# Kernel optimization log

Measured on AMD Instinct MI355X. Metric: run time of the kernel, lower is better.

The kernel has to match this reference:

```python
import jax, jax.numpy as jnp
import numpy as np

B, T = 4, 15
NY = NX = 256
RES = 0.05
LAT0 = 32.0
G = 9.81
F0 = 1e-4
C0 = 2.7
DT = 21600.0
TINT = 86400.0
NSTEP = int(TINT // DT)  # 4 Euler sub-steps

# --- grid spacing: mean of dx, dy as in lonlat2dxdy (uniform lon/lat grid) ---
_lat = LAT0 + RES * np.arange(NX, dtype=np.float64)  # lat varies along axis 1
_dx_mean = RES * 111000.0
_dy_mean = RES * 111000.0 * np.mean(np.cos(np.deg2rad(_lat)))
DX = np.float32(0.5 * (_dx_mean + _dy_mean))

# --- Helmholtz operator in DST-I space, shape (NY-2, NX-2) (square grid) ---
_i = np.arange(1, NX - 1, dtype=np.float64)
_j = np.arange(1, NY - 1, dtype=np.float64)
_X, _Y = np.meshgrid(_i, _j, indexing='ij')
_lap = (2 * (np.cos(np.pi / (NX - 1) * _X) - 1) / DX**2
        + 2 * (np.cos(np.pi / (NY - 1) * _Y) - 1) / DX**2)
HELM = jnp.asarray((G / F0) * _lap - G * F0 / C0**2, dtype=jnp.float32)

# --- boundary masks (SSH=None -> no NaN land mask; ind0 is empty) ---
_m = np.full((NY, NX), 3, dtype=np.int32)
_m[0, :] = _m[:, 0] = _m[-1, :] = _m[:, -1] = 1
_m[1, 1:-1] = 2; _m[1:-1, 1] = 2
_m[-2, 1:-1] = 2; _m[-3, 1:-1] = 2
_m[1:-1, -2] = 2; _m[1:-1, -3] = 2
IND12 = jnp.asarray((_m == 1) | (_m == 2))


def dstI1D(x):
    """1D type-I discrete sine transform along last axis."""
    n = x.shape[-1]
    xp = jnp.pad(x, [(0, 0)] * (x.ndim - 1) + [(1, 1)])
    return jnp.fft.irfft(-1j * xp, norm='ortho')[..., 1:n + 1]


def dstI2D(x):
    return jnp.swapaxes(dstI1D(jnp.swapaxes(dstI1D(x), -1, -2)), -1, -2)


def h2uv(h):
    """SSH -> geostrophic (u, v). f is the constant F0."""
    u = jnp.zeros_like(h).at[..., 1:-1, 1:].set(
        -G / F0 * (h[..., 2:, :-1] + h[..., 2:, 1:] - h[..., :-2, 1:] - h[..., :-2, :-1]) / (4 * DX))
    v = jnp.zeros_like(h).at[..., 1:, 1:-1].set(
        G / F0 * (h[..., 1:, 2:] + h[..., :-1, 2:] - h[..., :-1, :-2] - h[..., 1:, :-2]) / (4 * DX))
    return u, v


def h2pv(h, hbc):
    """SSH -> potential vorticity with boundary values from hbc on ind1|ind2."""
    interior = (G / F0 * ((h[..., 2:, 1:-1] + h[..., :-2, 1:-1] - 2 * h[..., 1:-1, 1:-1]) / DX**2
                          + (h[..., 1:-1, 2:] + h[..., 1:-1, :-2] - 2 * h[..., 1:-1, 1:-1]) / DX**2)
                - G * F0 / C0**2 * h[..., 1:-1, 1:-1])
    q = jnp.zeros_like(h).at[..., 1:-1, 1:-1].set(interior)
    return jnp.where(IND12, -G * F0 / C0**2 * hbc, q)


def _adv(up, vp, um, vm, v0):
    """3rd-order upwind advection."""
    c = 1.0 / (6 * DX)
    inner = (
        -up[..., 1:-1, 1:-1] * c * (2 * v0[..., 2:-2, 3:-1] + 3 * v0[..., 2:-2, 2:-2] - 6 * v0[..., 2:-2, 1:-3] + v0[..., 2:-2, :-4])
        + um[..., 1:-1, 1:-1] * c * (v0[..., 2:-2, 4:] - 6 * v0[..., 2:-2, 3:-1] + 3 * v0[..., 2:-2, 2:-2] + 2 * v0[..., 2:-2, 1:-3])
        - vp[..., 1:-1, 1:-1] * c * (2 * v0[..., 3:-1, 2:-2] + 3 * v0[..., 2:-2, 2:-2] - 6 * v0[..., 1:-3, 2:-2] + v0[..., :-4, 2:-2])
        + vm[..., 1:-1, 1:-1] * c * (v0[..., 4:, 2:-2] - 6 * v0[..., 3:-1, 2:-2] + 3 * v0[..., 2:-2, 2:-2] + 2 * v0[..., 1:-3, 2:-2]))
    return jnp.zeros_like(v0).at[..., 2:-2, 2:-2].set(inner)


def rhs(u, v, q0, way=1.0):
    uT = way * 0.5 * (u[..., 1:-1, 1:-1] + u[..., 1:-1, 2:])
    vT = way * 0.5 * (v[..., 1:-1, 1:-1] + v[..., 2:, 1:-1])
    up = jnp.maximum(uT, 0.0); um = jnp.minimum(uT, 0.0)
    vp = jnp.maximum(vT, 0.0); vm = jnp.minimum(vT, 0.0)
    r = _adv(up, vp, um, vm, q0)
    # beta term is identically zero: f = F0 is spatially constant. Kdiffus=None.
    return jnp.where(IND12, 0.0, r)


def pv2h(q, hb, qb):
    """PV -> SSH via DST-based inverse Helmholtz solve."""
    qin = q[..., 1:-1, 1:-1] - qb[..., 1:-1, 1:-1]
    inv = dstI2D(dstI2D(qin) / HELM)
    return jnp.zeros_like(q).at[..., 1:-1, 1:-1].set(inv) + hb


def conv2d(x, w, b):
    y = jax.lax.conv_general_dilated(x, w, (1, 1), 'SAME',
                                     dimension_numbers=('NCHW', 'OIHW', 'NCHW'))
    return y + b[None, :, None, None]


def qg_forecast(x):
    """One-day QG forecast of each frame from the previous one (NSTEP Euler sub-steps)."""
    h0 = x[:, :-1]            # [B, T-1, NY, NX]
    hb = h0                    # background / boundary SSH
    qb = h2pv(hb, hb)

    def body(carry, _):
        h, q = carry
        u, v = h2uv(h)
        q1 = q + DT * rhs(u, v, q)
        h1 = pv2h(q1, hb, qb)
        return (h1, q1), None

    (hf, _), _ = jax.lax.scan(body, (h0, qb), None, length=NSTEP)
    return hf


def setup_inputs() -> dict:
    key = jax.random.key(0)
    ks = jax.random.split(key, 8)
    s = 0.05
    return {
        'x': jax.random.normal(ks[0], (B, T, NY, NX), jnp.float32),
        'w_in': s * jax.random.normal(ks[1], (64, T, 3, 3), jnp.float32),
        'b_in': jnp.zeros((64,), jnp.float32),
        'w_hid': s * jax.random.normal(ks[2], (64, 64, 3, 3), jnp.float32),
        'b_hid': jnp.zeros((64,), jnp.float32),
        'w_b1': s * jax.random.normal(ks[3], (64, 64, 3, 3), jnp.float32),
        'b_b1': jnp.zeros((64,), jnp.float32),
        'w_b21': s * jax.random.normal(ks[4], (64, 64, 3, 3), jnp.float32),
        'b_b21': jnp.zeros((64,), jnp.float32),
        'w_b22': s * jax.random.normal(ks[5], (64, 64, 3, 3), jnp.float32),
        'b_b22': jnp.zeros((64,), jnp.float32),
        'w_out': s * jax.random.normal(ks[6], (T, 128, 3, 3), jnp.float32),
        'b_out': jnp.zeros((T,), jnp.float32),
    }


def reference(x, w_in, b_in, w_hid, b_hid, w_b1, b_b1, w_b21, b_b21,
              w_b22, b_b22, w_out, b_out):
    # QG dynamical prior cost
    hf = qg_forecast(x)
    dyn_cost = jnp.mean((x[:, 1:] - hf) ** 2)
    # bilinear AE prior cost (bilin_quad=False -> product of two branches)
    z = conv2d(x, w_in, b_in)
    z = conv2d(jax.nn.relu(z), w_hid, b_hid)
    nonlin = conv2d(z, w_b21, b_b21) * conv2d(z, w_b22, b_b22)
    xa = conv2d(jnp.concatenate([conv2d(z, w_b1, b_b1), nonlin], axis=1), w_out, b_out)
    ae_cost = jnp.mean((x - xa) ** 2)
    return dyn_cost + ae_cost
```

## Files before the change

kernel.cpp:

```cpp
#include <hip/hip_runtime.h>
#include <math.h>

#define NS 56
#define NPIX 65536

static constexpr double D_PI = 3.14159265358979323846;

typedef __attribute__((ext_vector_type(8))) short short8;
typedef __attribute__((ext_vector_type(4))) float f32x4;
typedef __attribute__((ext_vector_type(16))) float f32x16;

__device__ inline unsigned short f2bf(float f) {
  union { float f; unsigned int u; } v; v.f = f;
  unsigned int r = v.u + 0x7FFFu + ((v.u >> 16) & 1u);
  return (unsigned short)(r >> 16);
}
__device__ inline float bf2f(unsigned short b) {
  union { float f; unsigned int u; } v; v.u = ((unsigned int)b) << 16;
  return v.f;
}

#define SLC      (NS * NPIX)
#define OFF_PART 0
#define OFF_CNT  3584
#define OFF_S    4096
#define OFF_HM   36864
#define OFF_H    102400
#define OFF_QB   (OFF_H + SLC)
#define OFF_DQ0  (OFF_QB + SLC)
#define OFF_DQ1  (OFF_DQ0 + SLC / 2)
#define OFF_A1   (OFF_DQ1 + SLC / 2)
#define OFF_XP   (OFF_A1 + SLC / 2)
#define OFF_Z1   (OFF_XP + 2097152)
#define OFF_Z2   (OFF_Z1 + 8388608)
#define OFF_BC   (OFF_Z2 + 8388608)
#define OFF_XA   (OFF_BC + 8388608)
#define OFF_WT   (OFF_XA + 2097152)
#define W_IN    0
#define W_HID   10240
#define W_B1    47104
#define W_B21   83968
#define W_B22   120832
#define W_O1    157696
#define W_O2    166912

#define QCLAMP 1.0e12f
#define HCLAMP 1.0e15f

__global__ __launch_bounds__(256) void k_preamble(const float* __restrict__ x,
                                                  const float* __restrict__ w_in,
                                                  const float* __restrict__ w_hid,
                                                  const float* __restrict__ w_b1,
                                                  const float* __restrict__ w_b21,
                                                  const float* __restrict__ w_b22,
                                                  const float* __restrict__ w_out,
                                                  unsigned short* __restrict__ S,
                                                  float* __restrict__ HM,
                                                  unsigned short* __restrict__ wtb,
                                                  unsigned short* __restrict__ h,
                                                  unsigned short* __restrict__ qb,
                                                  unsigned short* __restrict__ xp,
                                                  unsigned int* __restrict__ cnt,
                                                  double* __restrict__ part,
                                                  float dx2, float gf, float gfc) {
  const int blk = blockIdx.x;
  const int tid = threadIdx.x;
  if (blk < 256) {
    int idx = blk * 256 + tid;
    if (idx == 0) *cnt = 0u;
    int i = idx >> 8, j = idx & 255;
    float sv = 0.f, hv = 1.f;
    if (i < 254 && j < 254) {
      double arg = D_PI * (double)((i + 1) * (j + 1)) / 255.0;
      sv = (float)((2.0 / sqrt(510.0)) * sin(arg));
      double la = 2.0 * (cos(D_PI * (double)(i + 1) / 255.0) - 1.0) / (double)dx2
                + 2.0 * (cos(D_PI * (double)(j + 1) / 255.0) - 1.0) / (double)dx2;
      hv = (float)((9.81 / 1e-4) * la - 9.81 * 1e-4 / (2.7 * 2.7));
    }
    S[idx] = f2bf(sv);
    HM[idx] = hv;
  } else if (blk < 256 + 1008) {
    int jb = blk - 256;
    int job = jb / 144;
    int e = (jb - job * 144) * 256 + tid;
    const float* src;
    int dstOff, chunks, icpShift, icw, ic0, icReal, ocw, ocReal;
    switch (job) {
      case 0: src = w_in;  dstOff = W_IN;  chunks = 5;  icpShift = 4; icw = 15;  ic0 = 0;  icReal = 15; ocw = 64; ocReal = 64; break;
      case 1: src = w_hid; dstOff = W_HID; chunks = 18; icpShift = 6; icw = 64;  ic0 = 0;  icReal = 64; ocw = 64; ocReal = 64; break;
      case 2: src = w_b1;  dstOff = W_B1;  chunks = 18; icpShift = 6; icw = 64;  ic0 = 0;  icReal = 64; ocw = 64; ocReal = 64; break;
      case 3: src = w_b21; dstOff = W_B21; chunks = 18; icpShift = 6; icw = 64;  ic0 = 0;  icReal = 64; ocw = 64; ocReal = 64; break;
      case 4: src = w_b22; dstOff = W_B22; chunks = 18; icpShift = 6; icw = 64;  ic0 = 0;  icReal = 64; ocw = 64; ocReal = 64; break;
      case 5: src = w_out; dstOff = W_O1;  chunks = 18; icpShift = 6; icw = 128; ic0 = 0;  icReal = 64; ocw = 16; ocReal = 15; break;
      default: src = w_out; dstOff = W_O2; chunks = 18; icpShift = 6; icw = 128; ic0 = 64; icReal = 64; ocw = 16; ocReal = 15; break;
    }
    int total = chunks * 4 * ocw * 8;
    if (e < total) {
      int j = e & 7;
      int oc = (e >> 3) % ocw;
      int ckg = e / (8 * ocw);
      int kg = ckg & 3, c = ckg >> 2;
      int Kidx = c * 32 + kg * 8 + j;
      int tap = Kidx >> icpShift;
      int ic = Kidx & ((1 << icpShift) - 1);
      float v = 0.f;
      if (tap < 9 && ic < icReal && oc < ocReal)
        v = src[((size_t)oc * icw + ic0 + ic) * 9 + tap];
      wtb[dstOff + e] = f2bf(v);
    }
  } else if (blk < 256 + 1008 + 14336) {
    int idx = (blk - 1264) * 256 + tid;
    int s = idx >> 16, p = idx & 65535;
    int y = p >> 8, xx = p & 255;
    int b = s / 14, t = s - b * 14;
    const float* hb = x + (size_t)(b * 15 + t) * NPIX;
    float hc = hb[p];
    float qv;
    if (y >= 2 && y <= 252 && xx >= 2 && xx <= 252) {
      qv = gf * ((hb[p + 256] + hb[p - 256] - 2.f * hc) / dx2
               + (hb[p + 1] + hb[p - 1] - 2.f * hc) / dx2) - gfc * hc;
    } else {
      qv = -gfc * hc;
    }
    h[idx] = f2bf(hc);
    qb[idx] = f2bf(qv);
  } else if (blk < 256 + 1008 + 14336 + 1024) {
    int e = (blk - 15600) * 256 + tid;
    int b = e >> 16, p = e & 65535;
    const float* xb = x + (size_t)b * 15 * NPIX + p;
    union { unsigned short u16[16]; uint4 u4[2]; } vv;
#pragma unroll
    for (int c = 0; c < 15; ++c) vv.u16[c] = f2bf(xb[(size_t)c * NPIX]);
    vv.u16[15] = 0;
    uint4* dst = (uint4*)&xp[(size_t)e * 16];
    dst[0] = vv.u4[0];
    dst[1] = vv.u4[1];
  } else {
    int s = blk - 16624;
    int b = s / 14, t = s - b * 14;
    const float* hb = x + (size_t)(b * 15 + t) * NPIX;
    const float* x1 = x + (size_t)(b * 15 + t + 1) * NPIX;
    double sum = 0.0;
    for (int i = tid; i < 1020; i += 256) {
      int y, xc;
      if (i < 256)      { y = 0;         xc = i; }
      else if (i < 512) { y = 255;       xc = i - 256; }
      else if (i < 766) { y = i - 511;   xc = 0; }
      else              { y = i - 765;   xc = 255; }
      int p = y * 256 + xc;
      float d = x1[p] - bf2f(f2bf(hb[p]));
      sum += (double)d * (double)d;
    }
    for (int o = 32; o > 0; o >>= 1) sum += __shfl_down(sum, o);
    __shared__ double sw[4];
    int lane = tid & 63, wid = tid >> 6;
    if (lane == 0) sw[wid] = sum;
    __syncthreads();
    if (tid == 0) part[1472 + s] = sw[0] + sw[1] + sw[2] + sw[3];
  }
}

template <bool FIRST>
__global__ __launch_bounds__(256) void k_qrhs_dq(const unsigned short* __restrict__ h,
                                                 const unsigned short* __restrict__ qbb,
                                                 const unsigned short* __restrict__ dqin,
                                                 unsigned short* __restrict__ dqout,
                                                 float ngf, float pgf, float fdx,
                                                 float cc, float dtf) {
  int idx = blockIdx.x * 256 + threadIdx.x;
  int s = idx >> 16, p = idx & 65535;
  int y = p >> 8, xx = p & 255;
  const unsigned short* H = h + (size_t)s * NPIX;
  const unsigned short* QB = qbb + (size_t)s * NPIX;
  const unsigned short* DQ = dqin + (size_t)s * NPIX;
  const int base = p - 257;
  auto dqv = [&](int d) -> float {
    if (FIRST) return 0.f;
    return bf2f(DQ[(base + d) & 65535]);
  };
  float q1mqb = 0.f;
  if (y >= 2 && y <= 252 && xx >= 2 && xx <= 252) {
    float hSW = bf2f(H[p + 255]), hS = bf2f(H[p + 256]), hSE = bf2f(H[p + 257]);
    float hNW = bf2f(H[p - 257]), hN = bf2f(H[p - 256]), hNE = bf2f(H[p - 255]);
    float hW = bf2f(H[p - 1]), hE = bf2f(H[p + 1]);
    float uA = ngf * (hSW + hS - hN - hNW) / fdx;
    float uB = ngf * (hS + hSE - hNE - hN) / fdx;
    float vA = pgf * (hE + hNE - hNW - hW) / fdx;
    float vB = pgf * (hSE + hE - hW - hSW) / fdx;
    float uT = 0.5f * (uA + uB);
    float vT = 0.5f * (vA + vB);
    float up = fmaxf(uT, 0.f), um = fminf(uT, 0.f);
    float vp = fmaxf(vT, 0.f), vm = fminf(vT, 0.f);
    float qbc = bf2f(QB[p]);
    float Q0 = qbc + dqv(0);
    float QE = bf2f(QB[p + 1]) + dqv(1), QW = bf2f(QB[p - 1]) + dqv(-1);
    float QEE = bf2f(QB[p + 2]) + dqv(2), QWW = bf2f(QB[p - 2]) + dqv(-2);
    float QS = bf2f(QB[p + 256]) + dqv(256), QN = bf2f(QB[p - 256]) + dqv(-256);
    float QSS = bf2f(QB[p + 512]) + dqv(512), QNN = bf2f(QB[p - 512]) + dqv(-512);
    float r = -up * cc * (2.f * QE + 3.f * Q0 - 6.f * QW + QWW)
            + um * cc * (QEE - 6.f * QE + 3.f * Q0 + 2.f * QW)
            - vp * cc * (2.f * QS + 3.f * Q0 - 6.f * QN + QNN)
            + vm * cc * (QSS - 6.f * QS + 3.f * Q0 + 2.f * QN);
    float q1 = Q0 + dtf * r;
    q1 = fminf(fmaxf(q1, -QCLAMP), QCLAMP);
    q1mqb = q1 - qbc;
  }
  int wy = (y == 0) ? 254 : ((y == 255) ? 255 : y - 1);
  int wx = (xx == 0) ? 254 : ((xx == 255) ? 255 : xx - 1);
  dqout[(size_t)s * NPIX + wy * 256 + wx] = f2bf(q1mqb);
}

__device__ inline f32x16 solve_core(const unsigned short* __restrict__ Sm,
                                    const unsigned short* __restrict__ X,
                                    unsigned short* __restrict__ Ul,
                                    int q, int w, int r31, int kh) {
  f32x16 acc;
#pragma unroll
  for (int i = 0; i < 16; ++i) acc[i] = 0.f;
  {
    const int ar = (32 * q + r31) * 256;
    const int br = (32 * w + r31) * 256;
#pragma unroll 4
    for (int kc = 0; kc < 256; kc += 16) {
      short8 a = *(const short8*)&Sm[ar + kc + kh * 8];
      short8 b = *(const short8*)&X[br + kc + kh * 8];
      acc = __builtin_amdgcn_mfma_f32_32x32x16_bf16(a, b, acc, 0, 0, 0);
    }
  }
  {
    const int col = 32 * w + r31;
    const int g = col >> 3, c7 = col & 7;
#pragma unroll
    for (int reg = 0; reg < 16; ++reg) {
      int i = (reg & 3) + 8 * (reg >> 2) + 4 * kh;
      Ul[i * 256 + (((g ^ (i & 7)) << 3) | c7)] = f2bf(acc[reg]);
    }
  }
  __syncthreads();
  f32x16 acc2;
#pragma unroll
  for (int i = 0; i < 16; ++i) acc2[i] = 0.f;
  {
    const int ar = (32 * w + r31) * 256;
    const int urow = r31 * 256;
    const int x7 = (r31 & 7);
#pragma unroll 4
    for (int kc = 0; kc < 256; kc += 16) {
      int g0 = (kc >> 3) + kh;
      short8 a = *(const short8*)&Sm[ar + kc + kh * 8];
      short8 b = *(const short8*)&Ul[urow + ((g0 ^ x7) << 3)];
      acc2 = __builtin_amdgcn_mfma_f32_32x32x16_bf16(a, b, acc2, 0, 0, 0);
    }
  }
  return acc2;
}

template <int EPI>
__global__ __launch_bounds__(512) void k_solve(const unsigned short* __restrict__ Sm,
                                               const unsigned short* __restrict__ Xb,
                                               unsigned short* __restrict__ Ob,
                                               const float* __restrict__ HM,
                                               const float* __restrict__ xin,
                                               unsigned short* __restrict__ hout,
                                               double* __restrict__ part) {
  __shared__ unsigned short Ul[32 * 256];
  const int s = blockIdx.x, q = blockIdx.y;
  const int lane = threadIdx.x & 63, w = threadIdx.x >> 6;
  const int r31 = lane & 31, kh = lane >> 5;
  f32x16 acc2 = solve_core(Sm, Xb + (size_t)s * NPIX, Ul, q, w, r31, kh);
  const int gn = 32 * q + r31;
  if (EPI == 0) {
    unsigned short* O = Ob + (size_t)s * NPIX;
#pragma unroll
    for (int reg = 0; reg < 16; ++reg) {
      int gm = 32 * w + (reg & 3) + 8 * (reg >> 2) + 4 * kh;
      O[(size_t)gm * 256 + gn] = f2bf(acc2[reg] / HM[(size_t)gm * 256 + gn]);
    }
  } else if (EPI == 1) {
    int b = s / 14, t = s - b * 14;
    const float* hb = xin + (size_t)(b * 15 + t) * NPIX;
    unsigned short* H = hout + (size_t)s * NPIX;
    if (gn < 254) {
#pragma unroll
      for (int reg = 0; reg < 16; ++reg) {
        int gm = 32 * w + (reg & 3) + 8 * (reg >> 2) + 4 * kh;
        if (gm < 254) {
          size_t o = (size_t)(gm + 1) * 256 + (gn + 1);
          float hv = acc2[reg] + hb[o];
          H[o] = f2bf(fminf(fmaxf(hv, -HCLAMP), HCLAMP));
        }
      }
    }
  } else {
    int b = s / 14, t = s - b * 14;
    const float* hb = xin + (size_t)(b * 15 + t) * NPIX;
    const float* x1 = xin + (size_t)(b * 15 + t + 1) * NPIX;
    double dsum = 0.0;
    if (gn < 254) {
#pragma unroll
      for (int reg = 0; reg < 16; ++reg) {
        int gm = 32 * w + (reg & 3) + 8 * (reg >> 2) + 4 * kh;
        if (gm < 254) {
          size_t o = (size_t)(gm + 1) * 256 + (gn + 1);
          float hv = acc2[reg] + hb[o];
          hv = fminf(fmaxf(hv, -HCLAMP), HCLAMP);
          float d = x1[o] - hv;
          dsum += (double)d * (double)d;
        }
      }
    }
    for (int o = 32; o > 0; o >>= 1) dsum += __shfl_down(dsum, o);
    __shared__ double sred[8];
    if (lane == 0) sred[w] = dsum;
    __syncthreads();
    if (threadIdx.x == 0) {
      double t8 = 0.0;
#pragma unroll
      for (int i = 0; i < 8; ++i) t8 += sred[i];
      part[1024 + s * 8 + q] = t8;
    }
  }
}

template <bool RELU>
__global__ __launch_bounds__(512) void k_conv64b(const unsigned short* __restrict__ in,
                                                 const unsigned short* __restrict__ wt,
                                                 const float* __restrict__ bias,
                                                 unsigned short* __restrict__ out) {
  __shared__ unsigned short tile[324 * 64];
  const int tid = threadIdx.x;
  const int lane = tid & 63, wave = tid >> 6;
  const int cl = lane & 15, kg = lane >> 4;
  const int wrow = wave & 3, wh = wave >> 2;
  const int b = blockIdx.z;
  const int gx0 = blockIdx.x * 16, gy0 = blockIdx.y * 16;

  f32x4 acc[4][2];
#pragma unroll
  for (int j = 0; j < 2; ++j) {
    float bv = bias[wh * 32 + j * 16 + cl];
#pragma unroll
    for (int i = 0; i < 4; ++i) acc[i][j] = (f32x4){bv, bv, bv, bv};
  }

  const unsigned short* inb = in + (size_t)b * NPIX * 64;
  for (int c = tid; c < 2592; c += 512) {
    int pp = c >> 3, g = c & 7;
    int ly = pp / 18, lx = pp - ly * 18;
    int iy = gy0 + ly - 1, ix = gx0 + lx - 1;
    uint4 v = make_uint4(0u, 0u, 0u, 0u);
    if (iy >= 0 && iy < 256 && ix >= 0 && ix < 256)
      v = *(const uint4*)&inb[((size_t)iy * 256 + ix) * 64 + g * 8];
    int sw = g ^ (pp & 7);
    *(uint4*)&tile[pp * 64 + sw * 8] = v;
  }
  __syncthreads();

#pragma unroll 3
  for (int cm = 0; cm < 18; ++cm) {
    const int tap = cm >> 1;
    const int g = (cm & 1) * 4 + kg;
    const int dy = tap / 3, dxx = tap - dy * 3;
    short8 bfr[2];
#pragma unroll
    for (int j = 0; j < 2; ++j)
      bfr[j] = *(const short8*)&wt[(((size_t)cm * 4 + kg) * 64 + wh * 32 + j * 16 + cl) * 8];
    const int tc = cl + dxx;
#pragma unroll
    for (int i = 0; i < 4; ++i) {
      int pp = (wrow * 4 + i + dy) * 18 + tc;
      int g2 = g ^ (pp & 7);
      short8 av = *(const short8*)&tile[pp * 64 + g2 * 8];
#pragma unroll
      for (int j = 0; j < 2; ++j)
        acc[i][j] = __builtin_amdgcn_mfma_f32_16x16x32_bf16(av, bfr[j], acc[i][j], 0, 0, 0);
    }
  }

  const size_t outBase = (size_t)b * NPIX * 64;
#pragma unroll
  for (int i = 0; i < 4; ++i) {
    int y = gy0 + wrow * 4 + i;
#pragma unroll
    for (int j = 0; j < 2; ++j) {
      int oc = wh * 32 + j * 16 + cl;
#pragma unroll
      for (int r = 0; r < 4; ++r) {
        int px = gx0 + kg * 4 + r;
        size_t oi = outBase + ((size_t)y * 256 + px) * 64 + oc;
        float v = acc[i][j][r];
        if (RELU) v = fmaxf(v, 0.f);
        out[oi] = f2bf(v);
      }
    }
  }
}

__global__ __launch_bounds__(512) void k_conv3(const unsigned short* __restrict__ in,
                                               const unsigned short* __restrict__ wt1,
                                               const unsigned short* __restrict__ wtA,
                                               const unsigned short* __restrict__ wtB,
                                               const float* __restrict__ bias1,
                                               const float* __restrict__ biasA,
                                               const float* __restrict__ biasB,
                                               unsigned short* __restrict__ out1,
                                               unsigned short* __restrict__ outm) {
  __shared__ unsigned short tile[324 * 64];
  const int tid = threadIdx.x;
  const int lane = tid & 63, wave = tid >> 6;
  const int cl = lane & 15, kg = lane >> 4;
  const int wrow = wave & 3, wh = wave >> 2;
  const int b = blockIdx.z;
  const int gx0 = blockIdx.x * 16, gy0 = blockIdx.y * 16;
  const size_t outBase = (size_t)b * NPIX * 64;

  const unsigned short* inb = in + (size_t)b * NPIX * 64;
  for (int c = tid; c < 2592; c += 512) {
    int pp = c >> 3, g = c & 7;
    int ly = pp / 18, lx = pp - ly * 18;
    int iy = gy0 + ly - 1, ix = gx0 + lx - 1;
    uint4 v = make_uint4(0u, 0u, 0u, 0u);
    if (iy >= 0 && iy < 256 && ix >= 0 && ix < 256)
      v = *(const uint4*)&inb[((size_t)iy * 256 + ix) * 64 + g * 8];
    int sw = g ^ (pp & 7);
    *(uint4*)&tile[pp * 64 + sw * 8] = v;
  }
  __syncthreads();

  {
    f32x4 acc[4][2];
#pragma unroll
    for (int j = 0; j < 2; ++j) {
      float bv = bias1[wh * 32 + j * 16 + cl];
#pragma unroll
      for (int i = 0; i < 4; ++i) acc[i][j] = (f32x4){bv, bv, bv, bv};
    }
#pragma unroll 3
    for (int cm = 0; cm < 18; ++cm) {
      const int tap = cm >> 1;
      const int g = (cm & 1) * 4 + kg;
      const int dy = tap / 3, dxx = tap - dy * 3;
      short8 bfr[2];
#pragma unroll
      for (int j = 0; j < 2; ++j)
        bfr[j] = *(const short8*)&wt1[(((size_t)cm * 4 + kg) * 64 + wh * 32 + j * 16 + cl) * 8];
      const int tc = cl + dxx;
#pragma unroll
      for (int i = 0; i < 4; ++i) {
        int pp = (wrow * 4 + i + dy) * 18 + tc;
        int g2 = g ^ (pp & 7);
        short8 av = *(const short8*)&tile[pp * 64 + g2 * 8];
#pragma unroll
        for (int j = 0; j < 2; ++j)
          acc[i][j] = __builtin_amdgcn_mfma_f32_16x16x32_bf16(av, bfr[j], acc[i][j], 0, 0, 0);
      }
    }
#pragma unroll
    for (int i = 0; i < 4; ++i) {
      int y = gy0 + wrow * 4 + i;
#pragma unroll
      for (int j = 0; j < 2; ++j) {
        int oc = wh * 32 + j * 16 + cl;
#pragma unroll
        for (int r = 0; r < 4; ++r) {
          int px = gx0 + kg * 4 + r;
          out1[outBase + ((size_t)y * 256 + px) * 64 + oc] = f2bf(acc[i][j][r]);
        }
      }
    }
  }

  {
    f32x4 accA[4][2], accB[4][2];
#pragma unroll
    for (int j = 0; j < 2; ++j) {
      float ba = biasA[wh * 32 + j * 16 + cl], bb = biasB[wh * 32 + j * 16 + cl];
#pragma unroll
      for (int i = 0; i < 4; ++i) {
        accA[i][j] = (f32x4){ba, ba, ba, ba};
        accB[i][j] = (f32x4){bb, bb, bb, bb};
      }
    }
#pragma unroll 2
    for (int cm = 0; cm < 18; ++cm) {
      const int tap = cm >> 1;
      const int g = (cm & 1) * 4 + kg;
      const int dy = tap / 3, dxx = tap - dy * 3;
      const int tc = cl + dxx;
      short8 wa[2], wb[2];
#pragma unroll
      for (int j = 0; j < 2; ++j) {
        wa[j] = *(const short8*)&wtA[(((size_t)cm * 4 + kg) * 64 + wh * 32 + j * 16 + cl) * 8];
        wb[j] = *(const short8*)&wtB[(((size_t)cm * 4 + kg) * 64 + wh * 32 + j * 16 + cl) * 8];
      }
#pragma unroll
      for (int i = 0; i < 4; ++i) {
        int pp = (wrow * 4 + i + dy) * 18 + tc;
        int g2 = g ^ (pp & 7);
        short8 av = *(const short8*)&tile[pp * 64 + g2 * 8];
#pragma unroll
        for (int j = 0; j < 2; ++j) {
          accA[i][j] = __builtin_amdgcn_mfma_f32_16x16x32_bf16(av, wa[j], accA[i][j], 0, 0, 0);
          accB[i][j] = __builtin_amdgcn_mfma_f32_16x16x32_bf16(av, wb[j], accB[i][j], 0, 0, 0);
        }
      }
    }
#pragma unroll
    for (int i = 0; i < 4; ++i) {
      int y = gy0 + wrow * 4 + i;
#pragma unroll
      for (int j = 0; j < 2; ++j) {
        int oc = wh * 32 + j * 16 + cl;
#pragma unroll
        for (int r = 0; r < 4; ++r) {
          int px = gx0 + kg * 4 + r;
          outm[outBase + ((size_t)y * 256 + px) * 64 + oc] = f2bf(accA[i][j][r] * accB[i][j][r]);
        }
      }
    }
  }
}

__global__ __launch_bounds__(512) void k_convout(const unsigned short* __restrict__ in0,
                                                 const unsigned short* __restrict__ in1,
                                                 const unsigned short* __restrict__ wt,
                                                 const float* __restrict__ bias,
                                                 unsigned short* __restrict__ out) {
  __shared__ unsigned short tile[324 * 64];
  const int tid = threadIdx.x;
  const int lane = tid & 63, wave = tid >> 6;
  const int cl = lane & 15, kg = lane >> 4;
  const int b = blockIdx.z;
  const int gx0 = blockIdx.x * 16, gy0 = blockIdx.y * 16;

  f32x4 acc[2];
  {
    float bv = (cl < 15) ? bias[cl] : 0.f;
    acc[0] = (f32x4){bv, bv, bv, bv};
    acc[1] = acc[0];
  }

  for (int src = 0; src < 2; ++src) {
    const unsigned short* inb = (src ? in1 : in0) + (size_t)b * NPIX * 64;
    const unsigned short* wtp = wt + src * 9216;
    if (src) __syncthreads();
    for (int c = tid; c < 2592; c += 512) {
      int pp = c >> 3, g = c & 7;
      int ly = pp / 18, lx = pp - ly * 18;
      int iy = gy0 + ly - 1, ix = gx0 + lx - 1;
      uint4 v = make_uint4(0u, 0u, 0u, 0u);
      if (iy >= 0 && iy < 256 && ix >= 0 && ix < 256)
        v = *(const uint4*)&inb[((size_t)iy * 256 + ix) * 64 + g * 8];
      int sw = g ^ (pp & 7);
      *(uint4*)&tile[pp * 64 + sw * 8] = v;
    }
    __syncthreads();
#pragma unroll 3
    for (int cm = 0; cm < 18; ++cm) {
      const int tap = cm >> 1;
      const int g = (cm & 1) * 4 + kg;
      const int dy = tap / 3, dxx = tap - dy * 3;
      short8 bfr = *(const short8*)&wtp[(((size_t)cm * 4 + kg) * 16 + cl) * 8];
      const int tc = cl + dxx;
#pragma unroll
      for (int i = 0; i < 2; ++i) {
        int pp = (wave * 2 + i + dy) * 18 + tc;
        int g2 = g ^ (pp & 7);
        short8 av = *(const short8*)&tile[pp * 64 + g2 * 8];
        acc[i] = __builtin_amdgcn_mfma_f32_16x16x32_bf16(av, bfr, acc[i], 0, 0, 0);
      }
    }
  }

  const size_t outBase = (size_t)b * NPIX * 16;
#pragma unroll
  for (int i = 0; i < 2; ++i) {
    int y = gy0 + wave * 2 + i;
#pragma unroll
    for (int r = 0; r < 4; ++r) {
      int px = gx0 + kg * 4 + r;
      size_t oi = outBase + ((size_t)y * 256 + px) * 16 + cl;
      out[oi] = f2bf(acc[i][r]);
    }
  }
}

__global__ __launch_bounds__(256) void k_conv16(const unsigned short* __restrict__ in,
                                                const unsigned short* __restrict__ wt,
                                                const float* __restrict__ bias,
                                                unsigned short* __restrict__ out) {
  __shared__ unsigned short wlds[10240];
  __shared__ unsigned short tile[324 * 16];

  const int tid = threadIdx.x;
  const int lane = tid & 63, wave = tid >> 6;
  const int cl = lane & 15, kg = lane >> 4;
  const int b = blockIdx.z;
  const int gx0 = blockIdx.x * 16, gy0 = blockIdx.y * 16;

  {
    uint4* wl = (uint4*)wlds;
    const uint4* wg = (const uint4*)wt;
    for (int i = tid; i < 1280; i += 256) wl[i] = wg[i];
  }
  const unsigned short* inb = in + (size_t)b * NPIX * 16;
  for (int c = tid; c < 648; c += 256) {
    int pp = c >> 1, g = c & 1;
    int ly = pp / 18, lx = pp - ly * 18;
    int iy = gy0 + ly - 1, ix = gx0 + lx - 1;
    uint4 v = make_uint4(0u, 0u, 0u, 0u);
    if (iy >= 0 && iy < 256 && ix >= 0 && ix < 256)
      v = *(const uint4*)&inb[((size_t)iy * 256 + ix) * 16 + g * 8];
    int sw = g ^ (pp & 1);
    *(uint4*)&tile[pp * 16 + sw * 8] = v;
  }
  __syncthreads();

  f32x4 acc[4][4];
#pragma unroll
  for (int j = 0; j < 4; ++j) {
    float bv = bias[j * 16 + cl];
#pragma unroll
    for (int i = 0; i < 4; ++i) acc[i][j] = (f32x4){bv, bv, bv, bv};
  }

#pragma unroll
  for (int c = 0; c < 5; ++c) {
    int tap = 2 * c + (kg >> 1);
    int dy = tap / 3, dxx = tap - dy * 3;
    int gidx = kg & 1;
    short8 bfr[4];
#pragma unroll
    for (int j = 0; j < 4; ++j)
      bfr[j] = *(const short8*)&wlds[((c * 4 + kg) * 64 + j * 16 + cl) * 8];
    int tc = cl + dxx;
#pragma unroll
    for (int i = 0; i < 4; ++i) {
      int tr = wave * 4 + i + dy;
      if (tr > 17) tr = 17;
      int pp = tr * 18 + tc;
      int g2 = gidx ^ (pp & 1);
      short8 av = *(const short8*)&tile[pp * 16 + g2 * 8];
#pragma unroll
      for (int j = 0; j < 4; ++j)
        acc[i][j] = __builtin_amdgcn_mfma_f32_16x16x32_bf16(av, bfr[j], acc[i][j], 0, 0, 0);
    }
  }

  const size_t outBase = (size_t)b * NPIX * 64;
#pragma unroll
  for (int i = 0; i < 4; ++i) {
    int y = gy0 + wave * 4 + i;
#pragma unroll
    for (int j = 0; j < 4; ++j) {
      int oc = j * 16 + cl;
#pragma unroll
      for (int r = 0; r < 4; ++r) {
        int px = gx0 + kg * 4 + r;
        size_t oi = outBase + ((size_t)y * 256 + px) * 64 + oc;
        out[oi] = f2bf(fmaxf(acc[i][j][r], 0.f));
      }
    }
  }
}

__global__ __launch_bounds__(256) void k_red_ae(const float* __restrict__ x,
                                                const unsigned short* __restrict__ xa,
                                                double* __restrict__ part,
                                                unsigned int* __restrict__ cnt,
                                                float* __restrict__ out) {
  const int NBT = 1024;
  const int bid = blockIdx.x;
  const int tid = threadIdx.x;
  const int e = bid * 256 + tid;
  const int b = e >> 16, p = e & 65535;
  union { unsigned short u16[16]; uint4 u4[2]; } vv;
  const uint4* xap = (const uint4*)&xa[(size_t)e * 16];
  vv.u4[0] = xap[0];
  vv.u4[1] = xap[1];
  const float* xb = x + (size_t)b * 15 * NPIX + p;
  double sum = 0.0;
#pragma unroll
  for (int c = 0; c < 15; ++c) {
    float d = xb[(size_t)c * NPIX] - bf2f(vv.u16[c]);
    sum += (double)d * (double)d;
  }
  for (int o = 32; o > 0; o >>= 1) sum += __shfl_down(sum, o);
  __shared__ double sw[4];
  __shared__ bool last;
  int lane = tid & 63, wid = tid >> 6;
  if (lane == 0) sw[wid] = sum;
  __syncthreads();
  if (tid == 0) {
    part[bid] = sw[0] + sw[1] + sw[2] + sw[3];
    __threadfence();
    unsigned int t = atomicAdd(cnt, 1u);
    last = (t == (unsigned)(NBT - 1));
  }
  __syncthreads();
  if (last) {
    __threadfence();
    double s1 = 0.0, s2 = 0.0;
    for (int i = tid; i < 504; i += 256) s1 += part[1024 + i];
    for (int i = tid; i < NBT; i += 256) s2 += part[i];
    for (int o = 32; o > 0; o >>= 1) {
      s1 += __shfl_down(s1, o);
      s2 += __shfl_down(s2, o);
    }
    __shared__ double a1[4], a2[4];
    if (lane == 0) { a1[wid] = s1; a2[wid] = s2; }
    __syncthreads();
    if (tid == 0) {
      double v = (a1[0] + a1[1] + a1[2] + a1[3]) / (double)(NS * NPIX)
               + (a2[0] + a2[1] + a2[2] + a2[3]) / (double)(60 * NPIX);
      if (!(v == v)) v = 0.0;
      if (v > 1.0e30) v = 1.0e30;
      if (v < -1.0e30) v = -1.0e30;
      out[0] = (float)v;
    }
  }
}

extern "C" void kernel_launch(void* const* d_in, const int* in_sizes, int n_in,
                              void* d_out, int out_size, void* d_ws, size_t ws_size,
                              hipStream_t stream) {
  (void)in_sizes; (void)n_in; (void)out_size; (void)ws_size;
  const float* x     = (const float*)d_in[0];
  const float* w_in  = (const float*)d_in[1];
  const float* b_in  = (const float*)d_in[2];
  const float* w_hid = (const float*)d_in[3];
  const float* b_hid = (const float*)d_in[4];
  const float* w_b1  = (const float*)d_in[5];
  const float* b_b1  = (const float*)d_in[6];
  const float* w_b21 = (const float*)d_in[7];
  const float* b_b21 = (const float*)d_in[8];
  const float* w_b22 = (const float*)d_in[9];
  const float* b_b22 = (const float*)d_in[10];
  const float* w_out = (const float*)d_in[11];
  const float* b_out = (const float*)d_in[12];
  float* ws = (float*)d_ws;
  float* out = (float*)d_out;

  double mc = 0.0;
  for (int k = 0; k < 256; ++k) mc += cos((32.0 + 0.05 * k) * D_PI / 180.0);
  mc /= 256.0;
  float DXf = (float)(0.5 * (5550.0 + 5550.0 * mc));
  float dx2 = DXf * DXf;
  float gf  = (float)(9.81 / 1e-4);
  float ngf = (float)(-9.81 / 1e-4);
  float gfc = (float)(9.81 * 1e-4 / (2.7 * 2.7));
  float fdx = 4.0f * DXf;
  float cc  = 1.0f / (6.0f * DXf);
  float dtf = 21600.0f;

  double* part = (double*)d_ws;
  unsigned int* cnt = (unsigned int*)(ws + OFF_CNT);
  unsigned short* S  = (unsigned short*)(ws + OFF_S);
  float* HM = ws + OFF_HM;
  unsigned short* h  = (unsigned short*)(ws + OFF_H);
  unsigned short* qb = (unsigned short*)(ws + OFF_QB);
  unsigned short* dq0 = (unsigned short*)(ws + OFF_DQ0);
  unsigned short* dq1 = (unsigned short*)(ws + OFF_DQ1);
  unsigned short* A1 = (unsigned short*)(ws + OFF_A1);
  unsigned short* xp = (unsigned short*)(ws + OFF_XP);
  unsigned short* z1 = (unsigned short*)(ws + OFF_Z1);
  unsigned short* z2 = (unsigned short*)(ws + OFF_Z2);
  unsigned short* bc = (unsigned short*)(ws + OFF_BC);
  unsigned short* xa = (unsigned short*)(ws + OFF_XA);
  unsigned short* wtb = (unsigned short*)(ws + OFF_WT);

  k_preamble<<<dim3(16680), dim3(256), 0, stream>>>(x, w_in, w_hid, w_b1, w_b21, w_b22,
                                                    w_out, S, HM, wtb, h, qb, xp, cnt,
                                                    part, dx2, gf, gfc);

  dim3 sg(56, 8);
  dim3 qg(NS * NPIX / 256);
  unsigned short* dqc = dq0;
  unsigned short* dqn = dq1;
  for (int step = 0; step < 4; ++step) {
    if (step == 0)
      k_qrhs_dq<true><<<qg, dim3(256), 0, stream>>>(h, qb, dq1, dqc, ngf, gf, fdx, cc, dtf);
    else {
      k_qrhs_dq<false><<<qg, dim3(256), 0, stream>>>(h, qb, dqc, dqn, ngf, gf, fdx, cc, dtf);
      unsigned short* tmp = dqc; dqc = dqn; dqn = tmp;
    }
    k_solve<0><<<sg, dim3(512), 0, stream>>>(S, dqc, A1, HM, nullptr, nullptr, part);
    if (step < 3)
      k_solve<1><<<sg, dim3(512), 0, stream>>>(S, A1, nullptr, nullptr, x, h, part);
    else
      k_solve<2><<<sg, dim3(512), 0, stream>>>(S, A1, nullptr, nullptr, x, nullptr, part);
  }

  dim3 cg4(16, 16, 4);
  k_conv16<<<cg4, dim3(256), 0, stream>>>(xp, wtb + W_IN, b_in, z1);
  k_conv64b<false><<<cg4, dim3(512), 0, stream>>>(z1, wtb + W_HID, b_hid, z2);
  k_conv3<<<cg4, dim3(512), 0, stream>>>(z2, wtb + W_B1, wtb + W_B21, wtb + W_B22,
                                         b_b1, b_b21, b_b22, z1, bc);
  k_convout<<<cg4, dim3(512), 0, stream>>>(z1, bc, wtb + W_O1, b_out, xa);

  k_red_ae<<<dim3(1024), dim3(256), 0, stream>>>(x, xa, part, cnt, out);
}
```

Measured before the change: 467.3 us.

## Switch 64-channel convs to 32x32x16 MFMA with per-wave two-row tiles

Rewrites the 64-in/64-out 3x3 convolution kernels (k_conv64b and k_conv3) to use 32x32x16 bf16 MFMA instead of 16x16x32. Each wave now computes two image rows across all 64 output channels, where before it covered four rows for half the channels. This is meant to cut LDS A-fragment reads and the number of weight loads per MFMA, since each wave reuses one A fragment across all output channels. The trade-off is larger f32x16 accumulators and a remapped output store pattern, which raises register pressure and may change store coalescing.

```diff
diff --git a/kernel.cpp b/kernel.cpp
--- a/kernel.cpp
+++ b/kernel.cpp
@@ -329,18 +329,17 @@
                                                  unsigned short* __restrict__ out) {
   __shared__ unsigned short tile[324 * 64];
   const int tid = threadIdx.x;
-  const int lane = tid & 63, wave = tid >> 6;
-  const int cl = lane & 15, kg = lane >> 4;
-  const int wrow = wave & 3, wh = wave >> 2;
+  const int lane = tid & 63, wv = tid >> 6;
+  const int p31 = lane & 31, kh = lane >> 5;
   const int b = blockIdx.z;
   const int gx0 = blockIdx.x * 16, gy0 = blockIdx.y * 16;
 
-  f32x4 acc[4][2];
+  f32x16 acc[2];
 #pragma unroll
   for (int j = 0; j < 2; ++j) {
-    float bv = bias[wh * 32 + j * 16 + cl];
-#pragma unroll
-    for (int i = 0; i < 4; ++i) acc[i][j] = (f32x4){bv, bv, bv, bv};
+    float bv = bias[j * 32 + p31];
+#pragma unroll
+    for (int i = 0; i < 16; ++i) acc[j][i] = bv;
   }
 
   const unsigned short* inb = in + (size_t)b * NPIX * 64;
@@ -356,42 +355,37 @@
   }
   __syncthreads();
 
-#pragma unroll 3
-  for (int cm = 0; cm < 18; ++cm) {
-    const int tap = cm >> 1;
-    const int g = (cm & 1) * 4 + kg;
+  const int pr = p31 >> 4, pc = p31 & 15;
+#pragma unroll 4
+  for (int cm = 0; cm < 36; ++cm) {
+    const int tap = cm >> 2, u = cm & 3;
     const int dy = tap / 3, dxx = tap - dy * 3;
+    const int cw = 2 * tap + (u >> 1);
+    const int kgb = (u & 1) * 2 + kh;
     short8 bfr[2];
 #pragma unroll
     for (int j = 0; j < 2; ++j)
-      bfr[j] = *(const short8*)&wt[(((size_t)cm * 4 + kg) * 64 + wh * 32 + j * 16 + cl) * 8];
-    const int tc = cl + dxx;
-#pragma unroll
-    for (int i = 0; i < 4; ++i) {
-      int pp = (wrow * 4 + i + dy) * 18 + tc;
-      int g2 = g ^ (pp & 7);
-      short8 av = *(const short8*)&tile[pp * 64 + g2 * 8];
-#pragma unroll
-      for (int j = 0; j < 2; ++j)
-        acc[i][j] = __builtin_amdgcn_mfma_f32_16x16x32_bf16(av, bfr[j], acc[i][j], 0, 0, 0);
-    }
+      bfr[j] = *(const short8*)&wt[(((size_t)cw * 4 + kgb) * 64 + j * 32 + p31) * 8];
+    const int pp = (2 * wv + pr + dy) * 18 + pc + dxx;
+    const int g2 = (2 * u + kh) ^ (pp & 7);
+    short8 av = *(const short8*)&tile[pp * 64 + g2 * 8];
+#pragma unroll
+    for (int j = 0; j < 2; ++j)
+      acc[j] = __builtin_amdgcn_mfma_f32_32x32x16_bf16(av, bfr[j], acc[j], 0, 0, 0);
   }
 
   const size_t outBase = (size_t)b * NPIX * 64;
 #pragma unroll
-  for (int i = 0; i < 4; ++i) {
-    int y = gy0 + wrow * 4 + i;
+  for (int reg = 0; reg < 16; ++reg) {
+    int px = (reg & 3) + 8 * (reg >> 2) + 4 * kh;
+    int y = gy0 + 2 * wv + (px >> 4);
+    int xc = gx0 + (px & 15);
+    size_t ob = outBase + ((size_t)y * 256 + xc) * 64;
 #pragma unroll
     for (int j = 0; j < 2; ++j) {
-      int oc = wh * 32 + j * 16 + cl;
-#pragma unroll
-      for (int r = 0; r < 4; ++r) {
-        int px = gx0 + kg * 4 + r;
-        size_t oi = outBase + ((size_t)y * 256 + px) * 64 + oc;
-        float v = acc[i][j][r];
-        if (RELU) v = fmaxf(v, 0.f);
-        out[oi] = f2bf(v);
-      }
+      float v = acc[j][reg];
+      if (RELU) v = fmaxf(v, 0.f);
+      out[ob + j * 32 + p31] = f2bf(v);
     }
   }
 }
@@ -407,12 +401,12 @@
                                                unsigned short* __restrict__ outm) {
   __shared__ unsigned short tile[324 * 64];
   const int tid = threadIdx.x;
-  const int lane = tid & 63, wave = tid >> 6;
-  const int cl = lane & 15, kg = lane >> 4;
-  const int wrow = wave & 3, wh = wave >> 2;
+  const int lane = tid & 63, wv = tid >> 6;
+  const int p31 = lane & 31, kh = lane >> 5;
   const int b = blockIdx.z;
   const int gx0 = blockIdx.x * 16, gy0 = blockIdx.y * 16;
   const size_t outBase = (size_t)b * NPIX * 64;
+  const int pr = p31 >> 4, pc = p31 & 15;
 
   const unsigned short* inb = in + (size_t)b * NPIX * 64;
   for (int c = tid; c < 2592; c += 512) {
@@ -428,95 +422,80 @@
   __syncthreads();
 
   {
-    f32x4 acc[4][2];
+    f32x16 acc[2];
 #pragma unroll
     for (int j = 0; j < 2; ++j) {
-      float bv = bias1[wh * 32 + j * 16 + cl];
-#pragma unroll
-      for (int i = 0; i < 4; ++i) acc[i][j] = (f32x4){bv, bv, bv, bv};
-    }
-#pragma unroll 3
-    for (int cm = 0; cm < 18; ++cm) {
-      const int tap = cm >> 1;
-      const int g = (cm & 1) * 4 + kg;
+      float bv = bias1[j * 32 + p31];
+#pragma unroll
+      for (int i = 0; i < 16; ++i) acc[j][i] = bv;
+    }
+#pragma unroll 4
+    for (int cm = 0; cm < 36; ++cm) {
+      const int tap = cm >> 2, u = cm & 3;
       const int dy = tap / 3, dxx = tap - dy * 3;
+      const int cw = 2 * tap + (u >> 1);
+      const int kgb = (u & 1) * 2 + kh;
       short8 bfr[2];
 #pragma unroll
       for (int j = 0; j < 2; ++j)
-        bfr[j] = *(const short8*)&wt1[(((size_t)cm * 4 + kg) * 64 + wh * 32 + j * 16 + cl) * 8];
-      const int tc = cl + dxx;
-#pragma unroll
-      for (int i = 0; i < 4; ++i) {
-        int pp = (wrow * 4 + i + dy) * 18 + tc;
-        int g2 = g ^ (pp & 7);
-        short8 av = *(const short8*)&tile[pp * 64 + g2 * 8];
-#pragma unroll
-        for (int j = 0; j < 2; ++j)
-          acc[i][j] = __builtin_amdgcn_mfma_f32_16x16x32_bf16(av, bfr[j], acc[i][j], 0, 0, 0);
+        bfr[j] = *(const short8*)&wt1[(((size_t)cw * 4 + kgb) * 64 + j * 32 + p31) * 8];
+      const int pp = (2 * wv + pr + dy) * 18 + pc + dxx;
+      const int g2 = (2 * u + kh) ^ (pp & 7);
+      short8 av = *(const short8*)&tile[pp * 64 + g2 * 8];
+#pragma unroll
+      for (int j = 0; j < 2; ++j)
+        acc[j] = __builtin_amdgcn_mfma_f32_32x32x16_bf16(av, bfr[j], acc[j], 0, 0, 0);
+    }
+#pragma unroll
+    for (int reg = 0; reg < 16; ++reg) {
+      int px = (reg & 3) + 8 * (reg >> 2) + 4 * kh;
+      int y = gy0 + 2 * wv + (px >> 4);
+      int xc = gx0 + (px & 15);
+      size_t ob = outBase + ((size_t)y * 256 + xc) * 64;
+#pragma unroll
+      for (int j = 0; j < 2; ++j)
+        out1[ob + j * 32 + p31] = f2bf(acc[j][reg]);
+    }
+  }
+
+  {
+    f32x16 accA[2], accB[2];
+#pragma unroll
+    for (int j = 0; j < 2; ++j) {
+      float ba = biasA[j * 32 + p31], bb = biasB[j * 32 + p31];
+#pragma unroll
+      for (int i = 0; i < 16; ++i) { accA[j][i] = ba; accB[j][i] = bb; }
+    }
+#pragma unroll 2
+    for (int cm = 0; cm < 36; ++cm) {
+      const int tap = cm >> 2, u = cm & 3;
+      const int dy = tap / 3, dxx = tap - dy * 3;
+      const int cw = 2 * tap + (u >> 1);
+      const int kgb = (u & 1) * 2 + kh;
+      short8 wa[2], wb[2];
+#pragma unroll
+      for (int j = 0; j < 2; ++j) {
+        wa[j] = *(const short8*)&wtA[(((size_t)cw * 4 + kgb) * 64 + j * 32 + p31) * 8];
+        wb[j] = *(const short8*)&wtB[(((size_t)cw * 4 + kgb) * 64 + j * 32 + p31) * 8];
       }
-    }
-#pragma unroll
-    for (int i = 0; i < 4; ++i) {
-      int y = gy0 + wrow * 4 + i;
+      const int pp = (2 * wv + pr + dy) * 18 + pc + dxx;
+      const int g2 = (2 * u + kh) ^ (pp & 7);
+      short8 av = *(const short8*)&tile[pp * 64 + g2 * 8];
 #pragma unroll
       for (int j = 0; j < 2; ++j) {
-        int oc = wh * 32 + j * 16 + cl;
-#pragma unroll
-        for (int r = 0; r < 4; ++r) {
-          int px = gx0 + kg * 4 + r;
-          out1[outBase + ((size_t)y * 256 + px) * 64 + oc] = f2bf(acc[i][j][r]);
-        }
+        accA[j] = __builtin_amdgcn_mfma_f32_32x32x16_bf16(av, wa[j], accA[j], 0, 0, 0);
+        accB[j] = __builtin_amdgcn_mfma_f32_32x32x16_bf16(av, wb[j], accB[j], 0, 0, 0);
       }
     }
-  }
-
-  {
-    f32x4 accA[4][2], accB[4][2];
-#pragma unroll
-    for (int j = 0; j < 2; ++j) {
-      float ba = biasA[wh * 32 + j * 16 + cl], bb = biasB[wh * 32 + j * 16 + cl];
-#pragma unroll
-      for (int i = 0; i < 4; ++i) {
-        accA[i][j] = (f32x4){ba, ba, ba, ba};
-        accB[i][j] = (f32x4){bb, bb, bb, bb};
-      }
-    }
-#pragma unroll 2
-    for (int cm = 0; cm < 18; ++cm) {
-      const int tap = cm >> 1;
-      const int g = (cm & 1) * 4 + kg;
-      const int dy = tap / 3, dxx = tap - dy * 3;
-      const int tc = cl + dxx;
-      short8 wa[2], wb[2];
-#pragma unroll
-      for (int j = 0; j < 2; ++j) {
-        wa[j] = *(const short8*)&wtA[(((size_t)cm * 4 + kg) * 64 + wh * 32 + j * 16 + cl) * 8];
-        wb[j] = *(const short8*)&wtB[(((size_t)cm * 4 + kg) * 64 + wh * 32 + j * 16 + cl) * 8];
-      }
-#pragma unroll
-      for (int i = 0; i < 4; ++i) {
-        int pp = (wrow * 4 + i + dy) * 18 + tc;
-        int g2 = g ^ (pp & 7);
-        short8 av = *(const short8*)&tile[pp * 64 + g2 * 8];
-#pragma unroll
-        for (int j = 0; j < 2; ++j) {
-          accA[i][j] = __builtin_amdgcn_mfma_f32_16x16x32_bf16(av, wa[j], accA[i][j], 0, 0, 0);
-          accB[i][j] = __builtin_amdgcn_mfma_f32_16x16x32_bf16(av, wb[j], accB[i][j], 0, 0, 0);
-        }
-      }
-    }
-#pragma unroll
-    for (int i = 0; i < 4; ++i) {
-      int y = gy0 + wrow * 4 + i;
-#pragma unroll
-      for (int j = 0; j < 2; ++j) {
-        int oc = wh * 32 + j * 16 + cl;
-#pragma unroll
-        for (int r = 0; r < 4; ++r) {
-          int px = gx0 + kg * 4 + r;
-          outm[outBase + ((size_t)y * 256 + px) * 64 + oc] = f2bf(accA[i][j][r] * accB[i][j][r]);
-        }
-      }
+#pragma unroll
+    for (int reg = 0; reg < 16; ++reg) {
+      int px = (reg & 3) + 8 * (reg >> 2) + 4 * kh;
+      int y = gy0 + 2 * wv + (px >> 4);
+      int xc = gx0 + (px & 15);
+      size_t ob = outBase + ((size_t)y * 256 + xc) * 64;
+#pragma unroll
+      for (int j = 0; j < 2; ++j)
+        outm[ob + j * 32 + p31] = f2bf(accA[j][reg] * accB[j][reg]);
     }
   }
 }
```

Result: slower. 515.1 us (+10.2%).
